# Kernel tuning notes

Measured on AMD Instinct MI355X. Metric: run time of the kernel, lower is better.

The kernel has to match this reference:

```python
import math
import jax, jax.numpy as jnp
import numpy as np

N_IMAGES = 32
TOTAL_Q = 2048
TOTAL_KV = 2048
Q_IN = 1024
KV_IN = Q_IN + 9
D_QK = 1024
D_V = 1024
N_HEADS = 16
TEMP = 1.0
SCALER = 1.0 / (TEMP * math.sqrt(D_QK // N_HEADS))


def _ragged_seg_ids(total, n_seg, seed):
    rng = np.random.default_rng(seed)
    lens = rng.multinomial(total - n_seg, np.ones(n_seg) / n_seg) + 1  # every segment nonempty
    return jnp.asarray(np.repeat(np.arange(n_seg), lens), dtype=jnp.int32)


def setup_inputs() -> dict:
    key = jax.random.key(0)
    ks = jax.random.split(key, 12)
    s = 0.02
    return {
        "A": jax.random.normal(ks[0], (TOTAL_Q, Q_IN), jnp.float32),
        "B0": jax.random.normal(ks[1], (TOTAL_KV, KV_IN), jnp.float32),
        "seg_q": _ragged_seg_ids(TOTAL_Q, N_IMAGES, 1),
        "seg_kv": _ragged_seg_ids(TOTAL_KV, N_IMAGES, 2),
        "Wq": jax.random.normal(ks[2], (Q_IN, D_QK), jnp.float32) * s,
        "bq": jax.random.normal(ks[3], (D_QK,), jnp.float32) * s,
        "Wk": jax.random.normal(ks[4], (KV_IN, D_QK), jnp.float32) * s,
        "bk": jax.random.normal(ks[5], (D_QK,), jnp.float32) * s,
        "Wv": jax.random.normal(ks[6], (KV_IN, D_V), jnp.float32) * s,
        "bv": jax.random.normal(ks[7], (D_V,), jnp.float32) * s,
        "Wf": jax.random.normal(ks[8], (D_V, Q_IN), jnp.float32) * s,
        "bf": jax.random.normal(ks[9], (Q_IN,), jnp.float32) * s,
    }


def reference(A, B0, seg_q, seg_kv, Wq, bq, Wk, bk, Wv, bv, Wf, bf):
    # Linear projections on packed rows
    q = (A @ Wq + bq).reshape(TOTAL_Q, N_HEADS, -1)     # [Nq, h, dqk]
    k = (B0 @ Wk + bk).reshape(TOTAL_KV, N_HEADS, -1)   # [Nk, h, dqk]
    v = (B0 @ Wv + bv).reshape(TOTAL_KV, N_HEADS, -1)   # [Nk, h, dv]
    # Per-segment attention expressed as a block mask (same math as the
    # original Python loop over splits)
    scores = jnp.einsum('ihd,khd->ihk', q, k) * SCALER  # [Nq, h, Nk]
    mask = (seg_q[:, None] == seg_kv[None, :])[:, None, :]  # [Nq, 1, Nk]
    neg = jnp.finfo(scores.dtype).min
    w = jax.nn.softmax(jnp.where(mask, scores, neg), axis=-1)
    wv = jnp.einsum('ihk,khd->ihd', w, v).reshape(TOTAL_Q, -1)  # [Nq, h*dv]
    return wv @ Wf + bf  # [Nq, q_in_dim]
```

## Files before the change

### kernel.cpp

```cpp
#include <hip/hip_runtime.h>
#include <hip/hip_bf16.h>
#include <math.h>

#define TOTAL_Q   2048
#define TOTAL_KV  2048
#define QIN       1024
#define KVIN      1033
#define KVIN_P    1056
#define DQK       1024
#define DV        1024
#define KVSTR     2048
#define SCALER    0.125f

typedef __bf16 bf16x8 __attribute__((ext_vector_type(8)));
typedef float  f32x4  __attribute__((ext_vector_type(4)));

__device__ __forceinline__ void glds16(const __hip_bfloat16* g, __bf16* l)
{
    __builtin_amdgcn_global_load_lds(
        (const __attribute__((address_space(1))) void*)g,
        (__attribute__((address_space(3))) void*)l,
        16, 0, 0);
}

__global__ __launch_bounds__(256)
void prep_k(const float* __restrict__ A,  const float* __restrict__ B0,
            const float* __restrict__ Wq, const float* __restrict__ Wk,
            const float* __restrict__ Wv, const float* __restrict__ Wf,
            __hip_bfloat16* __restrict__ Abf, __hip_bfloat16* __restrict__ B0bf,
            __hip_bfloat16* __restrict__ Wqt, __hip_bfloat16* __restrict__ Wkt,
            __hip_bfloat16* __restrict__ Wvt, __hip_bfloat16* __restrict__ Wft)
{
    const int b   = blockIdx.x;
    const int tid = threadIdx.x;

    if (b < 2048) {
        int i = (b * 256 + tid) * 4;
        float4 f = *(const float4*)(A + i);
        __hip_bfloat16 o[4] = { __float2bfloat16(f.x), __float2bfloat16(f.y),
                                __float2bfloat16(f.z), __float2bfloat16(f.w) };
        *(uint2*)(Abf + i) = *(const uint2*)o;
        return;
    }
    if (b < 4160) {
        int idx = ((b - 2048) * 256 + tid) * 4;
        int r = idx / KVIN_P, c = idx - r * KVIN_P;
        __hip_bfloat16 o[4];
        #pragma unroll
        for (int j = 0; j < 4; ++j)
            o[j] = __float2bfloat16((c + j < KVIN) ? B0[(size_t)r * KVIN + c + j] : 0.f);
        *(uint2*)(B0bf + idx) = *(const uint2*)o;
        return;
    }

    const float* W; __hip_bfloat16* Wt; int K, Kp, k0, n0;
    if (b < 6208) {
        int z = b - 4160;
        W  = (z >= 1024) ? Wf : Wq;
        Wt = (z >= 1024) ? Wft : Wqt;
        K = 1024; Kp = 1024;
        int rem = z & 1023;
        k0 = (rem & 31) * 32; n0 = (rem >> 5) * 32;
    } else {
        int z = b - 6208;
        W  = (z >= 1056) ? Wv : Wk;
        Wt = (z >= 1056) ? Wvt : Wkt;
        K = KVIN; Kp = KVIN_P;
        int rem = (z >= 1056) ? z - 1056 : z;
        k0 = (rem % 33) * 32; n0 = (rem / 33) * 32;
    }
    const int tx = tid & 31, ty = tid >> 5;
    __shared__ float tile[32][33];
    #pragma unroll
    for (int i = 0; i < 4; ++i) {
        int k = k0 + ty + i * 8;
        tile[ty + i * 8][tx] = (k < K) ? W[(size_t)k * 1024 + n0 + tx] : 0.f;
    }
    __syncthreads();
    #pragma unroll
    for (int i = 0; i < 4; ++i) {
        int n = n0 + ty + i * 8;
        Wt[(size_t)n * Kp + k0 + tx] = __float2bfloat16(tile[tx][ty + i * 8]);
    }
}

__global__ __launch_bounds__(256)
void gemm_qkv(const __hip_bfloat16* __restrict__ Abf,
              const __hip_bfloat16* __restrict__ Wqt,
              const float* __restrict__ bq,
              __hip_bfloat16* __restrict__ qb,
              const __hip_bfloat16* __restrict__ B0bf,
              const __hip_bfloat16* __restrict__ Wkvt,
              const float* __restrict__ bk, const float* __restrict__ bv,
              __hip_bfloat16* __restrict__ kvb)
{
    __shared__ __bf16 As[128 * 32];
    __shared__ __bf16 Bs[128 * 32];

    int b = blockIdx.x;
    const __hip_bfloat16 *Ag, *Btg; const float *bias0, *bias1;
    __hip_bfloat16* C; int N, K, bx, by;
    if (b < 128) {
        Ag = Abf; Btg = Wqt; bias0 = bq; bias1 = bq; C = qb;
        N = 1024; K = 1024; bx = b & 7; by = b >> 3;
    } else {
        b -= 128;
        Ag = B0bf; Btg = Wkvt; bias0 = bk; bias1 = bv; C = kvb;
        N = 2048; K = KVIN_P; bx = b & 15; by = b >> 4;
    }
    const int row0 = by * 128, col0 = bx * 128;

    const int tid  = threadIdx.x;
    const int wave = tid >> 6, lane = tid & 63;
    const int quad = lane >> 4, l16 = lane & 15;
    const int wm = (wave >> 1) * 64, wn = (wave & 1) * 64;

    const int cr = lane >> 2;
    const int cc = (lane & 3) * 8;

    const __hip_bfloat16* gsrc[4];
    __bf16* ldst[4];
    #pragma unroll
    for (int i = 0; i < 4; ++i) {
        int c = wave * 4 + i;
        if (c < 8) {
            gsrc[i] = Ag  + (size_t)(row0 + c * 16 + cr) * K + cc;
            ldst[i] = &As[c * 512];
        } else {
            gsrc[i] = Btg + (size_t)(col0 + (c - 8) * 16 + cr) * K + cc;
            ldst[i] = &Bs[(c - 8) * 512];
        }
    }

    f32x4 acc[4][4] = {};

    for (int k0 = 0; k0 < K; k0 += 32) {
        #pragma unroll
        for (int i = 0; i < 4; ++i)
            glds16(gsrc[i] + k0, ldst[i]);
        __syncthreads();

        bf16x8 af[4], bfr[4];
        #pragma unroll
        for (int mi = 0; mi < 4; ++mi)
            af[mi] = *(const bf16x8*)&As[(wm + mi * 16 + l16) * 32 + quad * 8];
        #pragma unroll
        for (int ni = 0; ni < 4; ++ni)
            bfr[ni] = *(const bf16x8*)&Bs[(wn + ni * 16 + l16) * 32 + quad * 8];

        #pragma unroll
        for (int mi = 0; mi < 4; ++mi)
            #pragma unroll
            for (int ni = 0; ni < 4; ++ni)
                acc[mi][ni] = __builtin_amdgcn_mfma_f32_16x16x32_bf16(
                    af[mi], bfr[ni], acc[mi][ni], 0, 0, 0);
        __syncthreads();
    }

    #pragma unroll
    for (int mi = 0; mi < 4; ++mi) {
        #pragma unroll
        for (int ni = 0; ni < 4; ++ni) {
            const int col = col0 + wn + ni * 16 + l16;
            const float bia = (col < 1024) ? bias0[col] : bias1[col - 1024];
            #pragma unroll
            for (int r = 0; r < 4; ++r) {
                const int row = row0 + wm + mi * 16 + quad * 4 + r;
                C[(size_t)row * N + col] = __float2bfloat16(acc[mi][ni][r] + bia);
            }
        }
    }
}

__global__ __launch_bounds__(256)
void gemm_out(const __hip_bfloat16* __restrict__ A,
              const __hip_bfloat16* __restrict__ Bt,
              const float* __restrict__ bias,
              float* __restrict__ C,
              int M, int N, int K)
{
    __shared__ __bf16 As[128 * 32];
    __shared__ __bf16 Bs[64 * 32];

    const int tid  = threadIdx.x;
    const int wave = tid >> 6, lane = tid & 63;
    const int quad = lane >> 4, l16 = lane & 15;
    const int wm = (wave >> 1) * 64;
    const int wn = (wave & 1) * 32;
    const int row0 = blockIdx.y * 128, col0 = blockIdx.x * 64;

    const int cr = lane >> 2;
    const int cc = (lane & 3) * 8;

    const __hip_bfloat16* ga0 = A  + (size_t)(row0 + (wave * 2 + 0) * 16 + cr) * K + cc;
    const __hip_bfloat16* ga1 = A  + (size_t)(row0 + (wave * 2 + 1) * 16 + cr) * K + cc;
    const __hip_bfloat16* gb0 = Bt + (size_t)(col0 + wave * 16 + cr) * K + cc;

    f32x4 acc[4][2] = {};

    for (int k0 = 0; k0 < K; k0 += 32) {
        glds16(ga0 + k0, &As[(wave * 2 + 0) * 512]);
        glds16(ga1 + k0, &As[(wave * 2 + 1) * 512]);
        glds16(gb0 + k0, &Bs[wave * 512]);
        __syncthreads();

        bf16x8 af[4], bfr[2];
        #pragma unroll
        for (int mi = 0; mi < 4; ++mi)
            af[mi] = *(const bf16x8*)&As[(wm + mi * 16 + l16) * 32 + quad * 8];
        #pragma unroll
        for (int ni = 0; ni < 2; ++ni)
            bfr[ni] = *(const bf16x8*)&Bs[(wn + ni * 16 + l16) * 32 + quad * 8];

        #pragma unroll
        for (int mi = 0; mi < 4; ++mi)
            #pragma unroll
            for (int ni = 0; ni < 2; ++ni)
                acc[mi][ni] = __builtin_amdgcn_mfma_f32_16x16x32_bf16(
                    af[mi], bfr[ni], acc[mi][ni], 0, 0, 0);
        __syncthreads();
    }

    #pragma unroll
    for (int mi = 0; mi < 4; ++mi) {
        #pragma unroll
        for (int ni = 0; ni < 2; ++ni) {
            const int col = col0 + wn + ni * 16 + l16;
            const float b = bias[col];
            #pragma unroll
            for (int r = 0; r < 4; ++r) {
                const int row = row0 + wm + mi * 16 + quad * 4 + r;
                C[(size_t)row * N + col] = acc[mi][ni][r] + b;
            }
        }
    }
}

#define CH 64

__global__ __launch_bounds__(256)
void attn_mfma(const __hip_bfloat16* __restrict__ qg,
               const __hip_bfloat16* __restrict__ kg,
               const __hip_bfloat16* __restrict__ vg,
               const int* __restrict__ seg_q, const int* __restrict__ seg_kv,
               __hip_bfloat16* __restrict__ wv)
{
    const int h = blockIdx.x & 15;
    const int s = blockIdx.x >> 4;

    __shared__ int sb[4];
    __shared__ __bf16 Ks[CH][72];
    __shared__ __bf16 Vt[64][CH + 8];
    __shared__ __bf16 Ps[4][16][CH + 8];

    if (threadIdx.x == 0) {
        int lo, hi;
        lo = 0; hi = TOTAL_Q;
        while (lo < hi) { int m = (lo + hi) >> 1; if (seg_q[m] <  s) lo = m + 1; else hi = m; }
        sb[0] = lo;
        hi = TOTAL_Q;
        while (lo < hi) { int m = (lo + hi) >> 1; if (seg_q[m] <= s) lo = m + 1; else hi = m; }
        sb[1] = lo;
        lo = 0; hi = TOTAL_KV;
        while (lo < hi) { int m = (lo + hi) >> 1; if (seg_kv[m] <  s) lo = m + 1; else hi = m; }
        sb[2] = lo;
        hi = TOTAL_KV;
        while (lo < hi) { int m = (lo + hi) >> 1; if (seg_kv[m] <= s) lo = m + 1; else hi = m; }
        sb[3] = lo;
    }
    __syncthreads();
    const int qbeg = sb[0], qend = sb[1], kbeg = sb[2], kend = sb[3];

    const int tid  = threadIdx.x;
    const int wave = tid >> 6, lane = tid & 63;
    const int quad = lane >> 4, l16 = lane & 15;

    for (int qt = qbeg; qt < qend; qt += 64) {
        const int qrow = qt + wave * 16 + l16;
        const int qrc  = min(qrow, qend - 1);
        bf16x8 qf[2];
        qf[0] = *(const bf16x8*)(qg + (size_t)qrc * DQK + h * 64 + quad * 8);
        qf[1] = *(const bf16x8*)(qg + (size_t)qrc * DQK + h * 64 + 32 + quad * 8);

        float m[4]  = { -1e30f, -1e30f, -1e30f, -1e30f };
        float l[4]  = { 0.f, 0.f, 0.f, 0.f };
        f32x4 acc[4] = {};

        for (int c0 = kbeg; c0 < kend; c0 += CH) {
            const int cl = min(CH, kend - c0);
            __syncthreads();

            #pragma unroll
            for (int it = 0; it < 2; ++it) {
                int e = (it * 256 + tid) * 8;
                int r = e >> 6, d = e & 63;
                bf16x8 z = {};
                if (r < cl)
                    z = *(const bf16x8*)(kg + (size_t)(c0 + r) * KVSTR + h * 64 + d);
                *(bf16x8*)&Ks[r][d] = z;
            }
            #pragma unroll
            for (int it = 0; it < 4; ++it) {
                int e = (it * 256 + tid) * 4;
                int r = e >> 6, d = e & 63;
                __bf16 t0 = 0, t1 = 0, t2 = 0, t3 = 0;
                if (r < cl) {
                    bf16x8 vv;
                    uint2 uu = *(const uint2*)(vg + (size_t)(c0 + r) * KVSTR + h * 64 + d);
                    *(uint2*)&vv = uu;
                    t0 = vv[0]; t1 = vv[1]; t2 = vv[2]; t3 = vv[3];
                }
                Vt[d + 0][r] = t0; Vt[d + 1][r] = t1;
                Vt[d + 2][r] = t2; Vt[d + 3][r] = t3;
            }
            __syncthreads();

            f32x4 sc[4];
            #pragma unroll
            for (int t = 0; t < 4; ++t) {
                bf16x8 b0 = *(const bf16x8*)&Ks[t * 16 + l16][quad * 8];
                bf16x8 b1 = *(const bf16x8*)&Ks[t * 16 + l16][32 + quad * 8];
                f32x4 z = {};
                z = __builtin_amdgcn_mfma_f32_16x16x32_bf16(qf[0], b0, z, 0, 0, 0);
                z = __builtin_amdgcn_mfma_f32_16x16x32_bf16(qf[1], b1, z, 0, 0, 0);
                sc[t] = z;
            }

            float sv[4][4];
            #pragma unroll
            for (int t = 0; t < 4; ++t) {
                const bool ok = (c0 + t * 16 + l16) < kend;
                #pragma unroll
                for (int r = 0; r < 4; ++r)
                    sv[t][r] = ok ? sc[t][r] * SCALER : -1e30f;
            }

            #pragma unroll
            for (int r = 0; r < 4; ++r) {
                float mx = fmaxf(fmaxf(sv[0][r], sv[1][r]), fmaxf(sv[2][r], sv[3][r]));
                mx = fmaxf(mx, __shfl_xor(mx, 1));
                mx = fmaxf(mx, __shfl_xor(mx, 2));
                mx = fmaxf(mx, __shfl_xor(mx, 4));
                mx = fmaxf(mx, __shfl_xor(mx, 8));
                const float mn = fmaxf(m[r], mx);
                const float alpha = __expf(m[r] - mn);
                m[r] = mn;
                float rs = 0.f;
                #pragma unroll
                for (int t = 0; t < 4; ++t) {
                    const float p = __expf(sv[t][r] - mn);
                    sv[t][r] = p;
                    rs += p;
                }
                rs += __shfl_xor(rs, 1);
                rs += __shfl_xor(rs, 2);
                rs += __shfl_xor(rs, 4);
                rs += __shfl_xor(rs, 8);
                l[r] = l[r] * alpha + rs;
                #pragma unroll
                for (int dt = 0; dt < 4; ++dt) acc[dt][r] *= alpha;
            }

            #pragma unroll
            for (int t = 0; t < 4; ++t)
                #pragma unroll
                for (int r = 0; r < 4; ++r)
                    Ps[wave][quad * 4 + r][t * 16 + l16] = (__bf16)sv[t][r];
            __syncthreads();

            #pragma unroll
            for (int ks = 0; ks < 2; ++ks) {
                bf16x8 pa = *(const bf16x8*)&Ps[wave][l16][ks * 32 + quad * 8];
                #pragma unroll
                for (int dt = 0; dt < 4; ++dt) {
                    bf16x8 vbf = *(const bf16x8*)&Vt[dt * 16 + l16][ks * 32 + quad * 8];
                    acc[dt] = __builtin_amdgcn_mfma_f32_16x16x32_bf16(pa, vbf, acc[dt], 0, 0, 0);
                }
            }
        }

        float inv[4];
        #pragma unroll
        for (int r = 0; r < 4; ++r) inv[r] = 1.f / l[r];
        #pragma unroll
        for (int dt = 0; dt < 4; ++dt) {
            #pragma unroll
            for (int r = 0; r < 4; ++r) {
                const int row = qt + wave * 16 + quad * 4 + r;
                if (row < qend)
                    wv[(size_t)row * DV + h * 64 + dt * 16 + l16] =
                        __float2bfloat16(acc[dt][r] * inv[r]);
            }
        }
    }
}

extern "C" void kernel_launch(void* const* d_in, const int* in_sizes, int n_in,
                              void* d_out, int out_size, void* d_ws, size_t ws_size,
                              hipStream_t stream)
{
    const float* A     = (const float*)d_in[0];
    const float* B0    = (const float*)d_in[1];
    const int*   seg_q = (const int*)  d_in[2];
    const int*   seg_kv= (const int*)  d_in[3];
    const float* Wq    = (const float*)d_in[4];
    const float* bq    = (const float*)d_in[5];
    const float* Wk    = (const float*)d_in[6];
    const float* bk    = (const float*)d_in[7];
    const float* Wv    = (const float*)d_in[8];
    const float* bv    = (const float*)d_in[9];
    const float* Wf    = (const float*)d_in[10];
    const float* bf    = (const float*)d_in[11];
    float* out = (float*)d_out;

    __hip_bfloat16* B0bf = (__hip_bfloat16*)d_ws;
    __hip_bfloat16* Wqt  = B0bf + (size_t)TOTAL_KV * KVIN_P;
    __hip_bfloat16* Wkt  = Wqt  + (size_t)QIN * DQK;
    __hip_bfloat16* Wvt  = Wkt  + (size_t)DQK * KVIN_P;
    __hip_bfloat16* Wft  = Wvt  + (size_t)DV * KVIN_P;
    __hip_bfloat16* Abf  = Wft  + (size_t)DV * QIN;
    __hip_bfloat16* qb   = Abf  + (size_t)TOTAL_Q * QIN;
    __hip_bfloat16* kvb  = qb   + (size_t)TOTAL_Q * DQK;
    __hip_bfloat16* wvb  = Abf;

    const dim3 b256(256);

    prep_k<<<dim3(8320), b256, 0, stream>>>(A, B0, Wq, Wk, Wv, Wf,
                                            Abf, B0bf, Wqt, Wkt, Wvt, Wft);

    gemm_qkv<<<dim3(384), b256, 0, stream>>>(Abf, Wqt, bq, qb,
                                             B0bf, Wkt, bk, bv, kvb);

    attn_mfma<<<dim3(32 * 16), b256, 0, stream>>>(qb, kvb, kvb + 1024, seg_q, seg_kv, wvb);

    gemm_out<<<dim3(QIN / 64, TOTAL_Q / 128), b256, 0, stream>>>(
        wvb, Wft, bf, out, TOTAL_Q, QIN, DV);
}
```

Measured before the change: 173.5 us.

## Shrink QKV GEMM tiles and split-K the output GEMM with atomics

The QKV projection tile width drops from 128 to 64 columns, which doubles the block count to 768 so more of the CUs have work. The output projection is split into two K halves that accumulate into the output with float atomicAdd. The bias is pre-written into the output by extra blocks in the prep kernel. This trades more parallel blocks for atomic traffic, less reuse per tile, and a nondeterministic summation order.

```diff
diff --git a/kernel.cpp b/kernel.cpp
--- a/kernel.cpp
+++ b/kernel.cpp
@@ -27,9 +27,11 @@
 void prep_k(const float* __restrict__ A,  const float* __restrict__ B0,
             const float* __restrict__ Wq, const float* __restrict__ Wk,
             const float* __restrict__ Wv, const float* __restrict__ Wf,
+            const float* __restrict__ bf,
             __hip_bfloat16* __restrict__ Abf, __hip_bfloat16* __restrict__ B0bf,
             __hip_bfloat16* __restrict__ Wqt, __hip_bfloat16* __restrict__ Wkt,
-            __hip_bfloat16* __restrict__ Wvt, __hip_bfloat16* __restrict__ Wft)
+            __hip_bfloat16* __restrict__ Wvt, __hip_bfloat16* __restrict__ Wft,
+            float* __restrict__ outp)
 {
     const int b   = blockIdx.x;
     const int tid = threadIdx.x;
@@ -50,6 +52,13 @@
         for (int j = 0; j < 4; ++j)
             o[j] = __float2bfloat16((c + j < KVIN) ? B0[(size_t)r * KVIN + c + j] : 0.f);
         *(uint2*)(B0bf + idx) = *(const uint2*)o;
+        return;
+    }
+    if (b >= 8320) {
+        int idx = ((b - 8320) * 256 + tid) * 4;
+        int c = idx & 1023;
+        float4 o = { bf[c], bf[c + 1], bf[c + 2], bf[c + 3] };
+        *(float4*)(outp + idx) = o;
         return;
     }
 
@@ -95,34 +104,34 @@
               __hip_bfloat16* __restrict__ kvb)
 {
     __shared__ __bf16 As[128 * 32];
-    __shared__ __bf16 Bs[128 * 32];
+    __shared__ __bf16 Bs[64 * 32];
 
     int b = blockIdx.x;
     const __hip_bfloat16 *Ag, *Btg; const float *bias0, *bias1;
     __hip_bfloat16* C; int N, K, bx, by;
-    if (b < 128) {
+    if (b < 256) {
         Ag = Abf; Btg = Wqt; bias0 = bq; bias1 = bq; C = qb;
-        N = 1024; K = 1024; bx = b & 7; by = b >> 3;
+        N = 1024; K = 1024; bx = b & 15; by = b >> 4;
     } else {
-        b -= 128;
+        b -= 256;
         Ag = B0bf; Btg = Wkvt; bias0 = bk; bias1 = bv; C = kvb;
-        N = 2048; K = KVIN_P; bx = b & 15; by = b >> 4;
-    }
-    const int row0 = by * 128, col0 = bx * 128;
+        N = 2048; K = KVIN_P; bx = b & 31; by = b >> 5;
+    }
+    const int row0 = by * 128, col0 = bx * 64;
 
     const int tid  = threadIdx.x;
     const int wave = tid >> 6, lane = tid & 63;
     const int quad = lane >> 4, l16 = lane & 15;
-    const int wm = (wave >> 1) * 64, wn = (wave & 1) * 64;
+    const int wm = (wave >> 1) * 64, wn = (wave & 1) * 32;
 
     const int cr = lane >> 2;
     const int cc = (lane & 3) * 8;
 
-    const __hip_bfloat16* gsrc[4];
-    __bf16* ldst[4];
-    #pragma unroll
-    for (int i = 0; i < 4; ++i) {
-        int c = wave * 4 + i;
+    const __hip_bfloat16* gsrc[3];
+    __bf16* ldst[3];
+    #pragma unroll
+    for (int i = 0; i < 3; ++i) {
+        int c = wave * 3 + i;
         if (c < 8) {
             gsrc[i] = Ag  + (size_t)(row0 + c * 16 + cr) * K + cc;
             ldst[i] = &As[c * 512];
@@ -132,26 +141,26 @@
         }
     }
 
-    f32x4 acc[4][4] = {};
+    f32x4 acc[4][2] = {};
 
     for (int k0 = 0; k0 < K; k0 += 32) {
         #pragma unroll
-        for (int i = 0; i < 4; ++i)
+        for (int i = 0; i < 3; ++i)
             glds16(gsrc[i] + k0, ldst[i]);
         __syncthreads();
 
-        bf16x8 af[4], bfr[4];
+        bf16x8 af[4], bfr[2];
         #pragma unroll
         for (int mi = 0; mi < 4; ++mi)
             af[mi] = *(const bf16x8*)&As[(wm + mi * 16 + l16) * 32 + quad * 8];
         #pragma unroll
-        for (int ni = 0; ni < 4; ++ni)
+        for (int ni = 0; ni < 2; ++ni)
             bfr[ni] = *(const bf16x8*)&Bs[(wn + ni * 16 + l16) * 32 + quad * 8];
 
         #pragma unroll
         for (int mi = 0; mi < 4; ++mi)
             #pragma unroll
-            for (int ni = 0; ni < 4; ++ni)
+            for (int ni = 0; ni < 2; ++ni)
                 acc[mi][ni] = __builtin_amdgcn_mfma_f32_16x16x32_bf16(
                     af[mi], bfr[ni], acc[mi][ni], 0, 0, 0);
         __syncthreads();
@@ -160,7 +169,7 @@
     #pragma unroll
     for (int mi = 0; mi < 4; ++mi) {
         #pragma unroll
-        for (int ni = 0; ni < 4; ++ni) {
+        for (int ni = 0; ni < 2; ++ni) {
             const int col = col0 + wn + ni * 16 + l16;
             const float bia = (col < 1024) ? bias0[col] : bias1[col - 1024];
             #pragma unroll
@@ -175,7 +184,6 @@
 __global__ __launch_bounds__(256)
 void gemm_out(const __hip_bfloat16* __restrict__ A,
               const __hip_bfloat16* __restrict__ Bt,
-              const float* __restrict__ bias,
               float* __restrict__ C,
               int M, int N, int K)
 {
@@ -188,20 +196,31 @@
     const int wm = (wave >> 1) * 64;
     const int wn = (wave & 1) * 32;
     const int row0 = blockIdx.y * 128, col0 = blockIdx.x * 64;
+    const int kz0 = blockIdx.z * (K / 2), kz1 = kz0 + K / 2;
 
     const int cr = lane >> 2;
     const int cc = (lane & 3) * 8;
 
-    const __hip_bfloat16* ga0 = A  + (size_t)(row0 + (wave * 2 + 0) * 16 + cr) * K + cc;
-    const __hip_bfloat16* ga1 = A  + (size_t)(row0 + (wave * 2 + 1) * 16 + cr) * K + cc;
-    const __hip_bfloat16* gb0 = Bt + (size_t)(col0 + wave * 16 + cr) * K + cc;
+    const __hip_bfloat16* gsrc[3];
+    __bf16* ldst[3];
+    #pragma unroll
+    for (int i = 0; i < 3; ++i) {
+        int c = wave * 3 + i;
+        if (c < 8) {
+            gsrc[i] = A  + (size_t)(row0 + c * 16 + cr) * K + cc;
+            ldst[i] = &As[c * 512];
+        } else {
+            gsrc[i] = Bt + (size_t)(col0 + (c - 8) * 16 + cr) * K + cc;
+            ldst[i] = &Bs[(c - 8) * 512];
+        }
+    }
 
     f32x4 acc[4][2] = {};
 
-    for (int k0 = 0; k0 < K; k0 += 32) {
-        glds16(ga0 + k0, &As[(wave * 2 + 0) * 512]);
-        glds16(ga1 + k0, &As[(wave * 2 + 1) * 512]);
-        glds16(gb0 + k0, &Bs[wave * 512]);
+    for (int k0 = kz0; k0 < kz1; k0 += 32) {
+        #pragma unroll
+        for (int i = 0; i < 3; ++i)
+            glds16(gsrc[i] + k0, ldst[i]);
         __syncthreads();
 
         bf16x8 af[4], bfr[2];
@@ -226,11 +245,10 @@
         #pragma unroll
         for (int ni = 0; ni < 2; ++ni) {
             const int col = col0 + wn + ni * 16 + l16;
-            const float b = bias[col];
             #pragma unroll
             for (int r = 0; r < 4; ++r) {
                 const int row = row0 + wm + mi * 16 + quad * 4 + r;
-                C[(size_t)row * N + col] = acc[mi][ni][r] + b;
+                atomicAdd(&C[(size_t)row * N + col], acc[mi][ni][r]);
             }
         }
     }
@@ -425,14 +443,14 @@
 
     const dim3 b256(256);
 
-    prep_k<<<dim3(8320), b256, 0, stream>>>(A, B0, Wq, Wk, Wv, Wf,
-                                            Abf, B0bf, Wqt, Wkt, Wvt, Wft);
-
-    gemm_qkv<<<dim3(384), b256, 0, stream>>>(Abf, Wqt, bq, qb,
+    prep_k<<<dim3(10368), b256, 0, stream>>>(A, B0, Wq, Wk, Wv, Wf, bf,
+                                             Abf, B0bf, Wqt, Wkt, Wvt, Wft, out);
+
+    gemm_qkv<<<dim3(768), b256, 0, stream>>>(Abf, Wqt, bq, qb,
                                              B0bf, Wkt, bk, bv, kvb);
 
     attn_mfma<<<dim3(32 * 16), b256, 0, stream>>>(qb, kvb, kvb + 1024, seg_q, seg_kv, wvb);
 
-    gemm_out<<<dim3(QIN / 64, TOTAL_Q / 128), b256, 0, stream>>>(
-        wvb, Wft, bf, out, TOTAL_Q, QIN, DV);
-}
+    gemm_out<<<dim3(QIN / 64, TOTAL_Q / 128, 2), b256, 0, stream>>>(
+        wvb, Wft, out, TOTAL_Q, QIN, DV);
+}
```

After: 173.0 us. Within noise of the previous version (-0.3%).
